# Kernel tuning notes

Measured on AMD Instinct MI355X. Metric: run time of the kernel, lower is better.

Reference implementation:

```python
import jax, jax.numpy as jnp
import numpy as np

N_HEADS = 16
D_HEAD = 64
TAU = 30.0
NEG = -1e9


def setup_inputs() -> dict:
    key = jax.random.key(0)
    k1, k2, k3, k4 = jax.random.split(key, 4)
    B, L, D = 2, 2048, 1024
    scale = 1.0 / np.sqrt(D)
    return {
        "input": jax.random.normal(k1, (B, L, D), dtype=jnp.float32),
        "attention_mask": jnp.ones((B, L), dtype=jnp.int32),
        "W_Q": jax.random.normal(k2, (N_HEADS * D_HEAD, D), dtype=jnp.float32) * scale,
        "W_K": jax.random.normal(k3, (N_HEADS * D_HEAD, D), dtype=jnp.float32) * scale,
        "W_V": jax.random.normal(k4, (N_HEADS * D_HEAD, D), dtype=jnp.float32) * scale,
    }


def reference(input, attention_mask, W_Q, W_K, W_V):
    B, L, D = input.shape
    # fused QKV projection (F.linear: x @ W.T), split into heads: [B, H, L, Dh]
    def proj(W):
        return jnp.einsum('bld,ed->ble', input, W).reshape(B, L, N_HEADS, D_HEAD).transpose(0, 2, 1, 3)
    q, k, v = proj(W_Q), proj(W_K), proj(W_V)
    S = jnp.einsum('bhqd,bhkd->bhqk', q, k) / np.sqrt(D_HEAD)  # [B,H,L,L]
    S = TAU * jnp.tanh(S)
    causal = jnp.tril(jnp.ones((L, L), dtype=bool))            # True = keep
    keep = causal[None, None, :, :] & (attention_mask[:, None, None, :] != 0)
    S = jnp.where(keep, S, NEG)
    attn = jax.nn.softmax(S, axis=-1)
    out = jnp.einsum('bhqk,bhkd->bhqd', attn, v)
    return out.transpose(0, 2, 1, 3).reshape(B, L, N_HEADS * D_HEAD)
```

## Files before the change

### kernel.cpp

```cpp
#include <hip/hip_runtime.h>
#include <hip/hip_bf16.h>


typedef unsigned short u16;
typedef __bf16 bf16x8 __attribute__((ext_vector_type(8)));
typedef float f32x4 __attribute__((ext_vector_type(4)));

#define MFMA(a, b, c) __builtin_amdgcn_mfma_f32_16x16x32_bf16(a, b, c, 0, 0, 0)

__device__ __forceinline__ u16 bf16rne(float f) {
    unsigned int u = __float_as_uint(f);
    u += 0x7fffu + ((u >> 16) & 1u);
    return (u16)(u >> 16);
}
__device__ __forceinline__ float bf16f(u16 h) {
    return __uint_as_float(((unsigned int)h) << 16);
}
__device__ __forceinline__ void split1(float f, u16& hi, u16& lo) {
    hi = bf16rne(f);
    lo = bf16rne(f - bf16f(hi));
}
__device__ __forceinline__ unsigned int pk2(float a, float b) {
    __hip_bfloat162 t = __float22bfloat162_rn(float2{a, b});
    return *(unsigned int*)&t;
}
__device__ __forceinline__ float fexp2(float x) {
#if __has_builtin(__builtin_amdgcn_exp2f)
    return __builtin_amdgcn_exp2f(x);
#else
    return __expf(x * 0.6931471805599453f);
#endif
}

__device__ __forceinline__ void gl16(const u16* g, u16* l) {
    __builtin_amdgcn_global_load_lds(
        (const __attribute__((address_space(1))) unsigned int*)g,
        (__attribute__((address_space(3))) unsigned int*)l, 16, 0, 0);
}

__global__ __launch_bounds__(256) void presplit(
    const float* __restrict__ X, const float* __restrict__ Wq,
    const float* __restrict__ Wk, const float* __restrict__ Wv,
    u16* __restrict__ Xh, u16* __restrict__ Xl,
    u16* __restrict__ Wqh, u16* __restrict__ Wql,
    u16* __restrict__ Wkh, u16* __restrict__ Wkl,
    u16* __restrict__ Wvh)
{
    int i = blockIdx.x * 256 + threadIdx.x;
    const float* src; u16 *dh, *dl; int off;
    if (i < 1048576)      { src = X;  dh = Xh;  dl = Xl;      off = i; }
    else if (i < 1310720) { src = Wq; dh = Wqh; dl = Wql;     off = i - 1048576; }
    else if (i < 1572864) { src = Wk; dh = Wkh; dl = Wkl;     off = i - 1310720; }
    else                  { src = Wv; dh = Wvh; dl = nullptr; off = i - 1572864; }
    float4 v = ((const float4*)src)[off];
    ushort4 h, l;
    split1(v.x, h.x, l.x); split1(v.y, h.y, l.y);
    split1(v.z, h.z, l.z); split1(v.w, h.w, l.w);
    ((ushort4*)dh)[off] = h;
    if (dl) ((ushort4*)dl)[off] = l;
}

__global__ __launch_bounds__(256, 3) void qkv_gemm(
    const u16* __restrict__ Xh, const u16* __restrict__ Xl,
    const u16* __restrict__ Wqh, const u16* __restrict__ Wql,
    const u16* __restrict__ Wkh, const u16* __restrict__ Wkl,
    const u16* __restrict__ Wvh,
    u16* __restrict__ Qh, u16* __restrict__ Ql,
    u16* __restrict__ Kh, u16* __restrict__ Kl,
    u16* __restrict__ VT)
{
    __shared__ __align__(16) u16 S[16384];
    u16* const Xhs = &S[0];
    u16* const Xls = &S[4096];
    u16* const Whs = &S[8192];
    u16* const Wls = &S[12288];
    const int tid = threadIdx.x;
    const int wave = tid >> 6, lane = tid & 63, quad = lane >> 4, c16 = lane & 15;
    const int id = blockIdx.x;
    const int nb = (((id >> 3) % 3) << 3) | (id & 7);
    const int m0 = ((id >> 3) / 3) * 128;
    const int mat = nb >> 3;
    const int n0 = (nb & 7) * 128;
    const u16* Bh = (mat == 0) ? Wqh : ((mat == 1) ? Wkh : Wvh);
    const u16* Bl = (mat == 0) ? Wql : Wkl;
    const int nseg = (mat < 2) ? 3 : 1;
    const int wm = (wave >> 1) * 64, wn = (wave & 1) * 64;

    const int srow0 = wave * 32 + (lane >> 2), scol = (lane & 3) * 8;

    f32x4 acc[4][4];
#pragma unroll
    for (int i = 0; i < 4; i++)
#pragma unroll
        for (int j = 0; j < 4; j++) acc[i][j] = (f32x4){0.f, 0.f, 0.f, 0.f};

    for (int kt = 0; kt < 32; kt++) {
        const int kcol = kt * 32;
#pragma unroll
        for (int s = 0; s < 2; s++) {
            int row = srow0 + s * 16;
            size_t go = (size_t)row * 1024 + kcol + scol;
            int lo = row * 32 + scol;
            gl16(Xh + (size_t)m0 * 1024 + go, &Xhs[lo]);
            gl16(Bh + (size_t)n0 * 1024 + go, &Whs[lo]);
            if (nseg == 3) {
                gl16(Xl + (size_t)m0 * 1024 + go, &Xls[lo]);
                gl16(Bl + (size_t)n0 * 1024 + go, &Wls[lo]);
            }
        }
        __syncthreads();
        bf16x8 xh[4], wh[4];
#pragma unroll
        for (int mt = 0; mt < 4; mt++)
            xh[mt] = *(const bf16x8*)&Xhs[(wm + mt * 16 + c16) * 32 + quad * 8];
#pragma unroll
        for (int nt = 0; nt < 4; nt++)
            wh[nt] = *(const bf16x8*)&Whs[(wn + nt * 16 + c16) * 32 + quad * 8];
#pragma unroll
        for (int mt = 0; mt < 4; mt++)
#pragma unroll
            for (int nt = 0; nt < 4; nt++)
                acc[mt][nt] = MFMA(xh[mt], wh[nt], acc[mt][nt]);
        if (nseg == 3) {
            bf16x8 wl[4];
#pragma unroll
            for (int nt = 0; nt < 4; nt++)
                wl[nt] = *(const bf16x8*)&Wls[(wn + nt * 16 + c16) * 32 + quad * 8];
#pragma unroll
            for (int mt = 0; mt < 4; mt++)
#pragma unroll
                for (int nt = 0; nt < 4; nt++)
                    acc[mt][nt] = MFMA(xh[mt], wl[nt], acc[mt][nt]);
            bf16x8 xl[4];
#pragma unroll
            for (int mt = 0; mt < 4; mt++)
                xl[mt] = *(const bf16x8*)&Xls[(wm + mt * 16 + c16) * 32 + quad * 8];
#pragma unroll
            for (int mt = 0; mt < 4; mt++)
#pragma unroll
                for (int nt = 0; nt < 4; nt++)
                    acc[mt][nt] = MFMA(xl[mt], wh[nt], acc[mt][nt]);
        }
        __syncthreads();
    }

    if (mat == 2) {
        u16* const T2 = &S[wave * 4096];
        const int nglob = n0 + wn + lane;
        const int hh = nglob >> 6, dh = nglob & 63;
        const int bh64 = ((m0 >> 11) * 16 + hh) * 64 + dh;
        u16* const vrow = VT + (size_t)bh64 * 2048 + (m0 & 2047) + wm;
#pragma unroll
        for (int half = 0; half < 2; half++) {
#pragma unroll
            for (int mt2 = 0; mt2 < 2; mt2++) {
                int mt = half * 2 + mt2;
#pragma unroll
                for (int nt = 0; nt < 4; nt++) {
                    uint2 d;
                    d.x = pk2(acc[mt][nt][0], acc[mt][nt][1]);
                    d.y = pk2(acc[mt][nt][2], acc[mt][nt][3]);
                    *(uint2*)&T2[(nt * 16 + c16) * 40 + mt2 * 16 + quad * 4] = d;
                }
            }
#pragma unroll
            for (int c = 0; c < 4; c++) {
                uint4 d = *(const uint4*)&T2[lane * 40 + c * 8];
                *(uint4*)&vrow[half * 32 + c * 8] = d;
            }
        }
    } else {
        const float scale = (mat == 0) ? 0.36067376022224085f : 1.f;
#pragma unroll
        for (int mt = 0; mt < 4; mt++) {
#pragma unroll
            for (int nt = 0; nt < 4; nt++) {
#pragma unroll
                for (int reg = 0; reg < 4; reg++) {
                    int mm = m0 + wm + mt * 16 + quad * 4 + reg;
                    int n = n0 + wn + nt * 16 + c16;
                    int b_ = mm >> 11, l = mm & 2047;
                    int h = n >> 6, dh = n & 63;
                    float v = acc[mt][nt][reg] * scale;
                    u16 hi, lo; split1(v, hi, lo);
                    int idx = ((b_ * 16 + h) * 2048 + l) * 64 + dh;
                    if (mat == 0) { Qh[idx] = hi; Ql[idx] = lo; }
                    else          { Kh[idx] = hi; Kl[idx] = lo; }
                }
            }
        }
    }
}

__global__ __launch_bounds__(256, 4) void attn(
    const u16* __restrict__ Qh, const u16* __restrict__ Ql,
    const u16* __restrict__ Kh, const u16* __restrict__ Kl,
    const u16* __restrict__ VT, const int* __restrict__ AM,
    u16* __restrict__ Op, float* __restrict__ Lp)
{
    __shared__ __align__(16) u16 Khs[2][4096];
    __shared__ __align__(16) u16 Kls[2][4096];
    __shared__ __align__(16) u16 Ps[4096];

    const int tid = threadIdx.x, wave = tid >> 6, lane = tid & 63;
    const int quad = lane >> 4, c16 = lane & 15;
    const int bh = blockIdx.x;
    const int pr = blockIdx.y;
    const int sp = blockIdx.z;
    const int b_ = bh >> 4;
    const size_t base = (size_t)bh * 2048 * 64;

    const int swsub[2] = { (wave * 2) >> 2, (wave * 2 + 1) >> 2 };
    const int swrow[2] = { ((wave * 2) & 3) * 16 + (lane >> 2), ((wave * 2 + 1) & 3) * 16 + (lane >> 2) };
    const int scol = (lane & 3) * 8;
    const int gscol = (((lane & 3) ^ ((lane >> 3) & 3))) * 8;
    const int rcsw = ((c16 >> 1) & 3) * 8;

    auto stageK = [&](int k0, int buf) {
        const u16* Kht = Kh + base + (size_t)k0 * 64;
        const u16* Klt = Kl + base + (size_t)k0 * 64;
#pragma unroll
        for (int s = 0; s < 2; s++) {
            int sub = swsub[s], row = swrow[s];
            int lo = sub * 2048 + row * 32 + scol;
            gl16(Kht + (size_t)row * 64 + sub * 32 + gscol, &Khs[buf][lo]);
            gl16(Klt + (size_t)row * 64 + sub * 32 + gscol, &Kls[buf][lo]);
        }
    };

    for (int tix = 0; tix < 2; ++tix) {
        const int qt = tix ? pr : 31 - pr;
        const int q0 = qt * 64;

        const size_t qrow = base + (size_t)(q0 + wave * 16 + c16) * 64 + quad * 8;
        bf16x8 qh0 = *(const bf16x8*)&Qh[qrow];
        bf16x8 qh1 = *(const bf16x8*)&Qh[qrow + 32];
        bf16x8 ql0 = *(const bf16x8*)&Ql[qrow];
        bf16x8 ql1 = *(const bf16x8*)&Ql[qrow + 32];

        float rsl[4] = {0.f, 0.f, 0.f, 0.f};
        f32x4 o[4];
#pragma unroll
        for (int r = 0; r < 4; r++) o[r] = (f32x4){0.f, 0.f, 0.f, 0.f};

        if (sp <= qt) {
            stageK(sp * 64, 0);
            int cur = 0;
            for (int kb = sp; kb <= qt; kb += 2) {
                const int k0 = kb * 64;
                __syncthreads();
                if (kb + 2 <= qt) stageK(k0 + 128, cur ^ 1);

                int mk[4];
#pragma unroll
                for (int nt = 0; nt < 4; nt++)
                    mk[nt] = AM[b_ * 2048 + k0 + nt * 16 + c16];
                bf16x8 vf[4][2];
#pragma unroll
                for (int dt = 0; dt < 4; dt++) {
                    const size_t vrow = (size_t)(bh * 64 + dt * 16 + c16) * 2048 + k0 + quad * 8;
                    vf[dt][0] = *(const bf16x8*)&VT[vrow];
                    vf[dt][1] = *(const bf16x8*)&VT[vrow + 32];
                }
                const bool interior = (kb < qt);

                float p[4][4];
#pragma unroll
                for (int nt = 0; nt < 4; nt++) {
                    const int krd = (nt * 16 + c16) * 32 + ((quad * 8) ^ rcsw);
                    bf16x8 kh0 = *(const bf16x8*)&Khs[cur][krd];
                    bf16x8 kh1 = *(const bf16x8*)&Khs[cur][2048 + krd];
                    bf16x8 kl0 = *(const bf16x8*)&Kls[cur][krd];
                    bf16x8 kl1 = *(const bf16x8*)&Kls[cur][2048 + krd];
                    f32x4 sa = (f32x4){0.f, 0.f, 0.f, 0.f};
                    sa = MFMA(qh0, kh0, sa);
                    sa = MFMA(qh1, kh1, sa);
                    sa = MFMA(ql0, kh0, sa);
                    sa = MFMA(ql1, kh1, sa);
                    sa = MFMA(qh0, kl0, sa);
                    sa = MFMA(qh1, kl1, sa);
                    const int key = k0 + nt * 16 + c16;
                    const bool mok = (mk[nt] != 0);
#pragma unroll
                    for (int reg = 0; reg < 4; reg++) {
                        int qg = q0 + wave * 16 + quad * 4 + reg;
                        float x = sa[reg];
                        float e1 = fexp2(x);
                        float r  = __builtin_amdgcn_rcpf(e1 + 1.f);
                        float pv = fexp2(-86.561702453337804f * r);
                        bool keep = mok && (interior || key <= qg);
                        pv = keep ? pv : 0.f;
                        p[nt][reg] = pv;
                        rsl[reg] += pv;
                    }
                }

#pragma unroll
                for (int nt = 0; nt < 4; nt++) {
                    int kl_ = nt * 16 + c16, sub = kl_ >> 5, kc = kl_ & 31;
#pragma unroll
                    for (int reg = 0; reg < 4; reg++)
                        Ps[sub * 2048 + (wave * 16 + quad * 4 + reg) * 32 + kc] = bf16rne(p[nt][reg]);
                }
                bf16x8 p0 = *(const bf16x8*)&Ps[(wave * 16 + c16) * 32 + quad * 8];
                bf16x8 p1 = *(const bf16x8*)&Ps[2048 + (wave * 16 + c16) * 32 + quad * 8];
#pragma unroll
                for (int dt = 0; dt < 4; dt++) {
                    o[dt] = MFMA(p0, vf[dt][0], o[dt]);
                    o[dt] = MFMA(p1, vf[dt][1], o[dt]);
                }
                cur ^= 1;
            }
        }
        __syncthreads();

        const size_t obase = (((size_t)sp * 1024 + (size_t)bh * 32 + qt) * 4096);
        const size_t lbase = (((size_t)sp * 1024 + (size_t)bh * 32 + qt) * 64);
        float lsum[4];
#pragma unroll
        for (int reg = 0; reg < 4; reg++) {
            float v = rsl[reg];
#pragma unroll
            for (int off = 1; off < 16; off <<= 1)
                v += __shfl_xor(v, off);
            lsum[reg] = v;
        }
        if (c16 == 0) {
#pragma unroll
            for (int reg = 0; reg < 4; reg++)
                Lp[lbase + wave * 16 + quad * 4 + reg] = lsum[reg];
        }
#pragma unroll
        for (int dt = 0; dt < 4; dt++)
#pragma unroll
            for (int reg = 0; reg < 4; reg++) {
                int row = wave * 16 + quad * 4 + reg;
                int d = dt * 16 + c16;
                Op[obase + row * 64 + d] = bf16rne(o[dt][reg]);
            }
    }
}

__global__ __launch_bounds__(256) void combine(
    const u16* __restrict__ Op, const float* __restrict__ Lp,
    float* __restrict__ Out)
{
    const int i = blockIdx.x * 256 + threadIdx.x;
    const size_t lin = (size_t)i * 4;
    const int d  = (int)(lin & 1023);
    const int h  = d >> 6, dd = d & 63;
    const int l  = (int)((lin >> 10) & 2047);
    const int b  = (int)(lin >> 21);
    const int qt = l >> 6, row = l & 63;
    const int bh = b * 16 + h;
    const size_t o0 = (((size_t)bh * 32 + qt) * 4096) + row * 64 + dd;
    const size_t o1 = o0 + (size_t)1024 * 4096;
    const size_t l0 = (((size_t)bh * 32 + qt) * 64) + row;
    ushort4 pa = *(const ushort4*)&Op[o0];
    ushort4 pb = *(const ushort4*)&Op[o1];
    float inv = __builtin_amdgcn_rcpf(Lp[l0] + Lp[l0 + 65536]);
    float4 r;
    r.x = (bf16f(pa.x) + bf16f(pb.x)) * inv;
    r.y = (bf16f(pa.y) + bf16f(pb.y)) * inv;
    r.z = (bf16f(pa.z) + bf16f(pb.z)) * inv;
    r.w = (bf16f(pa.w) + bf16f(pb.w)) * inv;
    *(float4*)&Out[lin] = r;
}

extern "C" void kernel_launch(void* const* d_in, const int* in_sizes, int n_in,
                              void* d_out, int out_size, void* d_ws, size_t ws_size,
                              hipStream_t stream) {
    const float* X  = (const float*)d_in[0];
    const int*   AM = (const int*)d_in[1];
    const float* Wq = (const float*)d_in[2];
    const float* Wk = (const float*)d_in[3];
    const float* Wv = (const float*)d_in[4];
    float* out = (float*)d_out;

    const size_t NE = (size_t)2 * 16 * 2048 * 64;
    const size_t WN = (size_t)1024 * 1024;
    u16* Qh  = (u16*)d_ws;
    u16* Ql  = Qh + NE;
    u16* Kh  = Ql + NE;
    u16* Kl  = Kh + NE;
    u16* VT  = Kl + NE;
    u16* Xh  = VT + NE;
    u16* Xl  = Xh + NE;
    u16* Wqh = Xl + NE;
    u16* Wql = Wqh + WN;
    u16* Wkh = Wql + WN;
    u16* Wkl = Wkh + WN;
    u16* Wvh = Wkl + WN;
    u16*   Op = Xh;
    float* Lp = (float*)Wqh;

    presplit<<<7168, 256, 0, stream>>>(X, Wq, Wk, Wv, Xh, Xl, Wqh, Wql, Wkh, Wkl, Wvh);
    qkv_gemm<<<768, 256, 0, stream>>>(Xh, Xl, Wqh, Wql, Wkh, Wkl, Wvh,
                                      Qh, Ql, Kh, Kl, VT);
    attn<<<dim3(32, 16, 2), 256, 0, stream>>>(Qh, Ql, Kh, Kl, VT, AM, Op, Lp);
    combine<<<4096, 256, 0, stream>>>(Op, Lp, out);
}
```

Measured before the change: 232.2 us.

## Double-buffer X tiles in LDS, load W fragments directly from global, swizzle LDS

The QKV GEMM now stages only the X hi/lo tiles through LDS, double-buffered, so the next k-tile's global-to-LDS copy overlaps the current tile's MFMAs. W fragments are read straight from global memory into registers rather than going through shared memory. An XOR swizzle on the LDS column index is meant to cut bank conflicts. The per-iteration sync structure changes, and per-lane uncoalesced global W reads may cost more bandwidth than they save.

```diff
diff --git a/kernel.cpp b/kernel.cpp
--- a/kernel.cpp
+++ b/kernel.cpp
@@ -70,10 +70,6 @@
     u16* __restrict__ VT)
 {
     __shared__ __align__(16) u16 S[16384];
-    u16* const Xhs = &S[0];
-    u16* const Xls = &S[4096];
-    u16* const Whs = &S[8192];
-    u16* const Wls = &S[12288];
     const int tid = threadIdx.x;
     const int wave = tid >> 6, lane = tid & 63, quad = lane >> 4, c16 = lane & 15;
     const int id = blockIdx.x;
@@ -86,46 +82,61 @@
     const int nseg = (mat < 2) ? 3 : 1;
     const int wm = (wave >> 1) * 64, wn = (wave & 1) * 64;
 
-    const int srow0 = wave * 32 + (lane >> 2), scol = (lane & 3) * 8;
-
-    f32x4 acc[4][4];
-#pragma unroll
-    for (int i = 0; i < 4; i++)
-#pragma unroll
-        for (int j = 0; j < 4; j++) acc[i][j] = (f32x4){0.f, 0.f, 0.f, 0.f};
-
-    for (int kt = 0; kt < 32; kt++) {
-        const int kcol = kt * 32;
+    const int srow0 = wave * 32 + (lane >> 2);
+    const int scol  = (lane & 3) * 8;
+    const int gscol = ((lane & 3) ^ ((lane >> 3) & 3)) * 8;
+    const int rsw   = ((c16 >> 1) & 3) * 8;
+
+    const u16* wbh = Bh + (size_t)(n0 + wn + c16) * 1024 + quad * 8;
+    const u16* wbl = Bl + (size_t)(n0 + wn + c16) * 1024 + quad * 8;
+
+    auto stageX = [&](int kt2, int buf) {
+        const int kcol = kt2 * 32;
 #pragma unroll
         for (int s = 0; s < 2; s++) {
             int row = srow0 + s * 16;
-            size_t go = (size_t)row * 1024 + kcol + scol;
-            int lo = row * 32 + scol;
-            gl16(Xh + (size_t)m0 * 1024 + go, &Xhs[lo]);
-            gl16(Bh + (size_t)n0 * 1024 + go, &Whs[lo]);
-            if (nseg == 3) {
-                gl16(Xl + (size_t)m0 * 1024 + go, &Xls[lo]);
-                gl16(Bl + (size_t)n0 * 1024 + go, &Wls[lo]);
-            }
-        }
-        __syncthreads();
-        bf16x8 xh[4], wh[4];
+            size_t go = (size_t)(m0 + row) * 1024 + kcol + gscol;
+            int lo = buf * 4096 + row * 32 + scol;
+            gl16(Xh + go, &S[lo]);
+            if (nseg == 3) gl16(Xl + go, &S[8192 + lo]);
+        }
+    };
+
+    f32x4 acc[4][4];
+#pragma unroll
+    for (int i = 0; i < 4; i++)
+#pragma unroll
+        for (int j = 0; j < 4; j++) acc[i][j] = (f32x4){0.f, 0.f, 0.f, 0.f};
+
+    stageX(0, 0);
+    __syncthreads();
+
+    for (int kt = 0; kt < 32; kt++) {
+        const int cur = kt & 1;
+        const int ko = kt * 32;
+
+        bf16x8 wh[4], wl[4];
+#pragma unroll
+        for (int nt = 0; nt < 4; nt++)
+            wh[nt] = *(const bf16x8*)&wbh[(size_t)nt * 16384 + ko];
+        if (nseg == 3) {
+#pragma unroll
+            for (int nt = 0; nt < 4; nt++)
+                wl[nt] = *(const bf16x8*)&wbl[(size_t)nt * 16384 + ko];
+        }
+
+        if (kt + 1 < 32) stageX(kt + 1, cur ^ 1);
+
+        bf16x8 xh[4];
 #pragma unroll
         for (int mt = 0; mt < 4; mt++)
-            xh[mt] = *(const bf16x8*)&Xhs[(wm + mt * 16 + c16) * 32 + quad * 8];
-#pragma unroll
-        for (int nt = 0; nt < 4; nt++)
-            wh[nt] = *(const bf16x8*)&Whs[(wn + nt * 16 + c16) * 32 + quad * 8];
+            xh[mt] = *(const bf16x8*)&S[cur * 4096 + (wm + mt * 16 + c16) * 32 + ((quad * 8) ^ rsw)];
 #pragma unroll
         for (int mt = 0; mt < 4; mt++)
 #pragma unroll
             for (int nt = 0; nt < 4; nt++)
                 acc[mt][nt] = MFMA(xh[mt], wh[nt], acc[mt][nt]);
         if (nseg == 3) {
-            bf16x8 wl[4];
-#pragma unroll
-            for (int nt = 0; nt < 4; nt++)
-                wl[nt] = *(const bf16x8*)&Wls[(wn + nt * 16 + c16) * 32 + quad * 8];
 #pragma unroll
             for (int mt = 0; mt < 4; mt++)
 #pragma unroll
@@ -134,7 +145,7 @@
             bf16x8 xl[4];
 #pragma unroll
             for (int mt = 0; mt < 4; mt++)
-                xl[mt] = *(const bf16x8*)&Xls[(wm + mt * 16 + c16) * 32 + quad * 8];
+                xl[mt] = *(const bf16x8*)&S[8192 + cur * 4096 + (wm + mt * 16 + c16) * 32 + ((quad * 8) ^ rsw)];
 #pragma unroll
             for (int mt = 0; mt < 4; mt++)
 #pragma unroll
```

Result: slower. 273.9 us (+18.0%).

## Fuse split-KV combine into attention via per-tile atomic ticket counters

Applied to the files above, without the earlier changes.

Removes the separate combine kernel. Each attention block now takes an atomic ticket for each of its query tiles after writing its partial output and row sums, and the second finisher of a tile combines both partials into the fp32 output. This saves one kernel launch and overlaps the combine with the tail of the attention work. In exchange it adds a memset of the ticket array, thread fences, atomics and extra block-level syncs at the end of every attention block.

```diff
diff --git a/kernel.cpp b/kernel.cpp
--- a/kernel.cpp
+++ b/kernel.cpp
@@ -196,11 +196,13 @@
     const u16* __restrict__ Qh, const u16* __restrict__ Ql,
     const u16* __restrict__ Kh, const u16* __restrict__ Kl,
     const u16* __restrict__ VT, const int* __restrict__ AM,
-    u16* __restrict__ Op, float* __restrict__ Lp)
+    u16* __restrict__ Op, float* __restrict__ Lp,
+    int* __restrict__ TK, float* __restrict__ Out)
 {
     __shared__ __align__(16) u16 Khs[2][4096];
     __shared__ __align__(16) u16 Kls[2][4096];
     __shared__ __align__(16) u16 Ps[4096];
+    __shared__ int bcast;
 
     const int tid = threadIdx.x, wave = tid >> 6, lane = tid & 63;
     const int quad = lane >> 4, c16 = lane & 15;
@@ -339,32 +341,39 @@
                 Op[obase + row * 64 + d] = bf16rne(o[dt][reg]);
             }
     }
-}
-
-__global__ __launch_bounds__(256) void combine(
-    const u16* __restrict__ Op, const float* __restrict__ Lp,
-    float* __restrict__ Out)
-{
-    const int i = blockIdx.x * 256 + threadIdx.x;
-    const size_t lin = (size_t)i * 4;
-    const int d  = (int)(lin & 1023);
-    const int h  = d >> 6, dd = d & 63;
-    const int l  = (int)((lin >> 10) & 2047);
-    const int b  = (int)(lin >> 21);
-    const int qt = l >> 6, row = l & 63;
-    const int bh = b * 16 + h;
-    const size_t o0 = (((size_t)bh * 32 + qt) * 4096) + row * 64 + dd;
-    const size_t o1 = o0 + (size_t)1024 * 4096;
-    const size_t l0 = (((size_t)bh * 32 + qt) * 64) + row;
-    ushort4 pa = *(const ushort4*)&Op[o0];
-    ushort4 pb = *(const ushort4*)&Op[o1];
-    float inv = __builtin_amdgcn_rcpf(Lp[l0] + Lp[l0 + 65536]);
-    float4 r;
-    r.x = (bf16f(pa.x) + bf16f(pb.x)) * inv;
-    r.y = (bf16f(pa.y) + bf16f(pb.y)) * inv;
-    r.z = (bf16f(pa.z) + bf16f(pb.z)) * inv;
-    r.w = (bf16f(pa.w) + bf16f(pb.w)) * inv;
-    *(float4*)&Out[lin] = r;
+
+    __threadfence();
+    __syncthreads();
+#pragma unroll
+    for (int tix = 0; tix < 2; ++tix) {
+        const int qt = tix ? pr : 31 - pr;
+        if (tid == 0) bcast = atomicAdd(&TK[bh * 32 + qt], 1);
+        __syncthreads();
+        const int win = bcast;
+        __syncthreads();
+        if (win == 1) {
+            __threadfence();
+            const int r = tid >> 2, c0 = (tid & 3) * 16;
+            const size_t t0 = ((size_t)bh * 32 + qt) * 4096 + r * 64 + c0;
+            const size_t l0 = ((size_t)bh * 32 + qt) * 64 + r;
+            const float inv = __builtin_amdgcn_rcpf(Lp[l0] + Lp[l0 + 65536]);
+            union { uint4 v[2]; u16 s[16]; } A, B2;
+            A.v[0]  = *(const uint4*)&Op[t0];
+            A.v[1]  = *(const uint4*)&Op[t0 + 8];
+            B2.v[0] = *(const uint4*)&Op[t0 + (size_t)1024 * 4096];
+            B2.v[1] = *(const uint4*)&Op[t0 + (size_t)1024 * 4096 + 8];
+            float* orow = Out + ((size_t)(b_ * 2048 + qt * 64 + r) * 1024) + (bh & 15) * 64 + c0;
+#pragma unroll
+            for (int g = 0; g < 4; g++) {
+                float4 w;
+                w.x = (bf16f(A.s[g * 4 + 0]) + bf16f(B2.s[g * 4 + 0])) * inv;
+                w.y = (bf16f(A.s[g * 4 + 1]) + bf16f(B2.s[g * 4 + 1])) * inv;
+                w.z = (bf16f(A.s[g * 4 + 2]) + bf16f(B2.s[g * 4 + 2])) * inv;
+                w.w = (bf16f(A.s[g * 4 + 3]) + bf16f(B2.s[g * 4 + 3])) * inv;
+                *(float4*)&orow[g * 4] = w;
+            }
+        }
+    }
 }
 
 extern "C" void kernel_launch(void* const* d_in, const int* in_sizes, int n_in,
@@ -393,10 +402,11 @@
     u16* Wvh = Wkl + WN;
     u16*   Op = Xh;
     float* Lp = (float*)Wqh;
+    int*   TK = (int*)(Wvh + WN);
 
     presplit<<<7168, 256, 0, stream>>>(X, Wq, Wk, Wv, Xh, Xl, Wqh, Wql, Wkh, Wkl, Wvh);
     qkv_gemm<<<768, 256, 0, stream>>>(Xh, Xl, Wqh, Wql, Wkh, Wkl, Wvh,
                                       Qh, Ql, Kh, Kl, VT);
-    attn<<<dim3(32, 16, 2), 256, 0, stream>>>(Qh, Ql, Kh, Kl, VT, AM, Op, Lp);
-    combine<<<4096, 256, 0, stream>>>(Op, Lp, out);
-}
+    hipMemsetAsync(TK, 0, 1024 * sizeof(int), stream);
+    attn<<<dim3(32, 16, 2), 256, 0, stream>>>(Qh, Ql, Kh, Kl, VT, AM, Op, Lp, TK, out);
+}
```

New measurement: 483.8 us. 108% more time.

## Drop split-K combine pass; one block per query tile with direct normalized output

Applied to the files above, without the earlier changes.

The attention kernel no longer splits keys across two blocks, pairs long and short query tiles, and merges partial results in a separate combine kernel. Each block now handles one query tile over all its keys, normalizes by the row sum and writes fp32 output directly. This removes the combine launch and the bf16 partial-output round trip. The low-part K tile is read straight from global into registers instead of shared memory, which shrinks LDS and raises the occupancy hint to 6. In exchange, the causal workload is no longer balanced across blocks, and the per-block serial loop is longer.

```diff
diff --git a/kernel.cpp b/kernel.cpp
--- a/kernel.cpp
+++ b/kernel.cpp
@@ -192,21 +192,20 @@
     }
 }
 
-__global__ __launch_bounds__(256, 4) void attn(
+__global__ __launch_bounds__(256, 6) void attn(
     const u16* __restrict__ Qh, const u16* __restrict__ Ql,
     const u16* __restrict__ Kh, const u16* __restrict__ Kl,
     const u16* __restrict__ VT, const int* __restrict__ AM,
-    u16* __restrict__ Op, float* __restrict__ Lp)
+    float* __restrict__ Out)
 {
     __shared__ __align__(16) u16 Khs[2][4096];
-    __shared__ __align__(16) u16 Kls[2][4096];
     __shared__ __align__(16) u16 Ps[4096];
 
     const int tid = threadIdx.x, wave = tid >> 6, lane = tid & 63;
     const int quad = lane >> 4, c16 = lane & 15;
     const int bh = blockIdx.x;
-    const int pr = blockIdx.y;
-    const int sp = blockIdx.z;
+    const int qt = 31 - blockIdx.y;
+    const int q0 = qt * 64;
     const int b_ = bh >> 4;
     const size_t base = (size_t)bh * 2048 * 64;
 
@@ -218,153 +217,116 @@
 
     auto stageK = [&](int k0, int buf) {
         const u16* Kht = Kh + base + (size_t)k0 * 64;
-        const u16* Klt = Kl + base + (size_t)k0 * 64;
 #pragma unroll
         for (int s = 0; s < 2; s++) {
             int sub = swsub[s], row = swrow[s];
-            int lo = sub * 2048 + row * 32 + scol;
-            gl16(Kht + (size_t)row * 64 + sub * 32 + gscol, &Khs[buf][lo]);
-            gl16(Klt + (size_t)row * 64 + sub * 32 + gscol, &Kls[buf][lo]);
+            gl16(Kht + (size_t)row * 64 + sub * 32 + gscol,
+                 &Khs[buf][sub * 2048 + row * 32 + scol]);
         }
     };
 
-    for (int tix = 0; tix < 2; ++tix) {
-        const int qt = tix ? pr : 31 - pr;
-        const int q0 = qt * 64;
-
-        const size_t qrow = base + (size_t)(q0 + wave * 16 + c16) * 64 + quad * 8;
-        bf16x8 qh0 = *(const bf16x8*)&Qh[qrow];
-        bf16x8 qh1 = *(const bf16x8*)&Qh[qrow + 32];
-        bf16x8 ql0 = *(const bf16x8*)&Ql[qrow];
-        bf16x8 ql1 = *(const bf16x8*)&Ql[qrow + 32];
-
-        float rsl[4] = {0.f, 0.f, 0.f, 0.f};
-        f32x4 o[4];
-#pragma unroll
-        for (int r = 0; r < 4; r++) o[r] = (f32x4){0.f, 0.f, 0.f, 0.f};
-
-        if (sp <= qt) {
-            stageK(sp * 64, 0);
-            int cur = 0;
-            for (int kb = sp; kb <= qt; kb += 2) {
-                const int k0 = kb * 64;
-                __syncthreads();
-                if (kb + 2 <= qt) stageK(k0 + 128, cur ^ 1);
-
-                int mk[4];
-#pragma unroll
-                for (int nt = 0; nt < 4; nt++)
-                    mk[nt] = AM[b_ * 2048 + k0 + nt * 16 + c16];
-                bf16x8 vf[4][2];
-#pragma unroll
-                for (int dt = 0; dt < 4; dt++) {
-                    const size_t vrow = (size_t)(bh * 64 + dt * 16 + c16) * 2048 + k0 + quad * 8;
-                    vf[dt][0] = *(const bf16x8*)&VT[vrow];
-                    vf[dt][1] = *(const bf16x8*)&VT[vrow + 32];
-                }
-                const bool interior = (kb < qt);
-
-                float p[4][4];
-#pragma unroll
-                for (int nt = 0; nt < 4; nt++) {
-                    const int krd = (nt * 16 + c16) * 32 + ((quad * 8) ^ rcsw);
-                    bf16x8 kh0 = *(const bf16x8*)&Khs[cur][krd];
-                    bf16x8 kh1 = *(const bf16x8*)&Khs[cur][2048 + krd];
-                    bf16x8 kl0 = *(const bf16x8*)&Kls[cur][krd];
-                    bf16x8 kl1 = *(const bf16x8*)&Kls[cur][2048 + krd];
-                    f32x4 sa = (f32x4){0.f, 0.f, 0.f, 0.f};
-                    sa = MFMA(qh0, kh0, sa);
-                    sa = MFMA(qh1, kh1, sa);
-                    sa = MFMA(ql0, kh0, sa);
-                    sa = MFMA(ql1, kh1, sa);
-                    sa = MFMA(qh0, kl0, sa);
-                    sa = MFMA(qh1, kl1, sa);
-                    const int key = k0 + nt * 16 + c16;
-                    const bool mok = (mk[nt] != 0);
-#pragma unroll
-                    for (int reg = 0; reg < 4; reg++) {
-                        int qg = q0 + wave * 16 + quad * 4 + reg;
-                        float x = sa[reg];
-                        float e1 = fexp2(x);
-                        float r  = __builtin_amdgcn_rcpf(e1 + 1.f);
-                        float pv = fexp2(-86.561702453337804f * r);
-                        bool keep = mok && (interior || key <= qg);
-                        pv = keep ? pv : 0.f;
-                        p[nt][reg] = pv;
-                        rsl[reg] += pv;
-                    }
-                }
-
-#pragma unroll
-                for (int nt = 0; nt < 4; nt++) {
-                    int kl_ = nt * 16 + c16, sub = kl_ >> 5, kc = kl_ & 31;
-#pragma unroll
-                    for (int reg = 0; reg < 4; reg++)
-                        Ps[sub * 2048 + (wave * 16 + quad * 4 + reg) * 32 + kc] = bf16rne(p[nt][reg]);
-                }
-                bf16x8 p0 = *(const bf16x8*)&Ps[(wave * 16 + c16) * 32 + quad * 8];
-                bf16x8 p1 = *(const bf16x8*)&Ps[2048 + (wave * 16 + c16) * 32 + quad * 8];
-#pragma unroll
-                for (int dt = 0; dt < 4; dt++) {
-                    o[dt] = MFMA(p0, vf[dt][0], o[dt]);
-                    o[dt] = MFMA(p1, vf[dt][1], o[dt]);
-                }
-                cur ^= 1;
-            }
-        }
+    const size_t qrow = base + (size_t)(q0 + wave * 16 + c16) * 64 + quad * 8;
+    bf16x8 qh0 = *(const bf16x8*)&Qh[qrow];
+    bf16x8 qh1 = *(const bf16x8*)&Qh[qrow + 32];
+    bf16x8 ql0 = *(const bf16x8*)&Ql[qrow];
+    bf16x8 ql1 = *(const bf16x8*)&Ql[qrow + 32];
+
+    float rsl[4] = {0.f, 0.f, 0.f, 0.f};
+    f32x4 o[4];
+#pragma unroll
+    for (int r = 0; r < 4; r++) o[r] = (f32x4){0.f, 0.f, 0.f, 0.f};
+
+    stageK(0, 0);
+    int cur = 0;
+    for (int kb = 0; kb <= qt; kb++) {
+        const int k0 = kb * 64;
         __syncthreads();
-
-        const size_t obase = (((size_t)sp * 1024 + (size_t)bh * 32 + qt) * 4096);
-        const size_t lbase = (((size_t)sp * 1024 + (size_t)bh * 32 + qt) * 64);
-        float lsum[4];
+        if (kb + 1 <= qt) stageK(k0 + 64, cur ^ 1);
+
+        int mk[4];
+#pragma unroll
+        for (int nt = 0; nt < 4; nt++)
+            mk[nt] = AM[b_ * 2048 + k0 + nt * 16 + c16];
+        bf16x8 vf[4][2];
+#pragma unroll
+        for (int dt = 0; dt < 4; dt++) {
+            const size_t vrow = (size_t)(bh * 64 + dt * 16 + c16) * 2048 + k0 + quad * 8;
+            vf[dt][0] = *(const bf16x8*)&VT[vrow];
+            vf[dt][1] = *(const bf16x8*)&VT[vrow + 32];
+        }
+        bf16x8 klf[4][2];
+#pragma unroll
+        for (int nt = 0; nt < 4; nt++) {
+            const size_t krow = base + (size_t)(k0 + nt * 16 + c16) * 64 + quad * 8;
+            klf[nt][0] = *(const bf16x8*)&Kl[krow];
+            klf[nt][1] = *(const bf16x8*)&Kl[krow + 32];
+        }
+        const bool interior = (kb < qt);
+
+        float p[4][4];
+#pragma unroll
+        for (int nt = 0; nt < 4; nt++) {
+            const int krd = (nt * 16 + c16) * 32 + ((quad * 8) ^ rcsw);
+            bf16x8 kh0 = *(const bf16x8*)&Khs[cur][krd];
+            bf16x8 kh1 = *(const bf16x8*)&Khs[cur][2048 + krd];
+            f32x4 sa = (f32x4){0.f, 0.f, 0.f, 0.f};
+            sa = MFMA(qh0, kh0, sa);
+            sa = MFMA(qh1, kh1, sa);
+            sa = MFMA(ql0, kh0, sa);
+            sa = MFMA(ql1, kh1, sa);
+            sa = MFMA(qh0, klf[nt][0], sa);
+            sa = MFMA(qh1, klf[nt][1], sa);
+            const int key = k0 + nt * 16 + c16;
+            const bool mok = (mk[nt] != 0);
+#pragma unroll
+            for (int reg = 0; reg < 4; reg++) {
+                int qg = q0 + wave * 16 + quad * 4 + reg;
+                float x = sa[reg];
+                float e1 = fexp2(x);
+                float r  = __builtin_amdgcn_rcpf(e1 + 1.f);
+                float pv = fexp2(-86.561702453337804f * r);
+                bool keep = mok && (interior || key <= qg);
+                pv = keep ? pv : 0.f;
+                p[nt][reg] = pv;
+                rsl[reg] += pv;
+            }
+        }
+
+#pragma unroll
+        for (int nt = 0; nt < 4; nt++) {
+            int kl_ = nt * 16 + c16, sub = kl_ >> 5, kc = kl_ & 31;
+#pragma unroll
+            for (int reg = 0; reg < 4; reg++)
+                Ps[sub * 2048 + (wave * 16 + quad * 4 + reg) * 32 + kc] = bf16rne(p[nt][reg]);
+        }
+        bf16x8 p0 = *(const bf16x8*)&Ps[(wave * 16 + c16) * 32 + quad * 8];
+        bf16x8 p1 = *(const bf16x8*)&Ps[2048 + (wave * 16 + c16) * 32 + quad * 8];
+#pragma unroll
+        for (int dt = 0; dt < 4; dt++) {
+            o[dt] = MFMA(p0, vf[dt][0], o[dt]);
+            o[dt] = MFMA(p1, vf[dt][1], o[dt]);
+        }
+        cur ^= 1;
+    }
+
+    float inv[4];
+#pragma unroll
+    for (int reg = 0; reg < 4; reg++) {
+        float v = rsl[reg];
+#pragma unroll
+        for (int off = 1; off < 16; off <<= 1)
+            v += __shfl_xor(v, off);
+        inv[reg] = __builtin_amdgcn_rcpf(v);
+    }
+    const int h = bh & 15;
+#pragma unroll
+    for (int dt = 0; dt < 4; dt++)
 #pragma unroll
         for (int reg = 0; reg < 4; reg++) {
-            float v = rsl[reg];
-#pragma unroll
-            for (int off = 1; off < 16; off <<= 1)
-                v += __shfl_xor(v, off);
-            lsum[reg] = v;
-        }
-        if (c16 == 0) {
-#pragma unroll
-            for (int reg = 0; reg < 4; reg++)
-                Lp[lbase + wave * 16 + quad * 4 + reg] = lsum[reg];
-        }
-#pragma unroll
-        for (int dt = 0; dt < 4; dt++)
-#pragma unroll
-            for (int reg = 0; reg < 4; reg++) {
-                int row = wave * 16 + quad * 4 + reg;
-                int d = dt * 16 + c16;
-                Op[obase + row * 64 + d] = bf16rne(o[dt][reg]);
-            }
-    }
-}
-
-__global__ __launch_bounds__(256) void combine(
-    const u16* __restrict__ Op, const float* __restrict__ Lp,
-    float* __restrict__ Out)
-{
-    const int i = blockIdx.x * 256 + threadIdx.x;
-    const size_t lin = (size_t)i * 4;
-    const int d  = (int)(lin & 1023);
-    const int h  = d >> 6, dd = d & 63;
-    const int l  = (int)((lin >> 10) & 2047);
-    const int b  = (int)(lin >> 21);
-    const int qt = l >> 6, row = l & 63;
-    const int bh = b * 16 + h;
-    const size_t o0 = (((size_t)bh * 32 + qt) * 4096) + row * 64 + dd;
-    const size_t o1 = o0 + (size_t)1024 * 4096;
-    const size_t l0 = (((size_t)bh * 32 + qt) * 64) + row;
-    ushort4 pa = *(const ushort4*)&Op[o0];
-    ushort4 pb = *(const ushort4*)&Op[o1];
-    float inv = __builtin_amdgcn_rcpf(Lp[l0] + Lp[l0 + 65536]);
-    float4 r;
-    r.x = (bf16f(pa.x) + bf16f(pb.x)) * inv;
-    r.y = (bf16f(pa.y) + bf16f(pb.y)) * inv;
-    r.z = (bf16f(pa.z) + bf16f(pb.z)) * inv;
-    r.w = (bf16f(pa.w) + bf16f(pb.w)) * inv;
-    *(float4*)&Out[lin] = r;
+            int row = q0 + wave * 16 + quad * 4 + reg;
+            Out[((size_t)(b_ * 2048 + row)) * 1024 + h * 64 + dt * 16 + c16]
+                = o[dt][reg] * inv[reg];
+        }
 }
 
 extern "C" void kernel_launch(void* const* d_in, const int* in_sizes, int n_in,
@@ -391,12 +353,9 @@
     u16* Wkh = Wql + WN;
     u16* Wkl = Wkh + WN;
     u16* Wvh = Wkl + WN;
-    u16*   Op = Xh;
-    float* Lp = (float*)Wqh;
 
     presplit<<<7168, 256, 0, stream>>>(X, Wq, Wk, Wv, Xh, Xl, Wqh, Wql, Wkh, Wkl, Wvh);
     qkv_gemm<<<768, 256, 0, stream>>>(Xh, Xl, Wqh, Wql, Wkh, Wkl, Wvh,
                                       Qh, Ql, Kh, Kl, VT);
-    attn<<<dim3(32, 16, 2), 256, 0, stream>>>(Qh, Ql, Kh, Kl, VT, AM, Op, Lp);
-    combine<<<4096, 256, 0, stream>>>(Op, Lp, out);
-}
+    attn<<<dim3(32, 32), 256, 0, stream>>>(Qh, Ql, Kh, Kl, VT, AM, out);
+}
```

Result: slower. 355.1 us (+52.9%).
